# Kernel tuning notes

Hardware: AMD Instinct MI355X
Metric: run time of the kernel (lower is better)

The kernel has to match this reference:

```python
import jax, jax.numpy as jnp
import numpy as np
from jax import lax


def _c1x1(t, w, b=None):
    # t: [B,C,H,W], w: [O,C] (1x1 conv == channel matmul)
    y = jnp.einsum('bchw,oc->bohw', t, w)
    if b is not None:
        y = y + b[None, :, None, None]
    return y


def _mamba(u, in_w, conv_w, conv_b, xproj_w, dt_w, dt_b, A_log, Dp, out_w):
    # u: [B,L,d_model]; Mamba block (mamba_ssm defaults: in/out/x_proj bias=False)
    B, L, _ = u.shape
    d_inner = conv_w.shape[0]
    d_state = A_log.shape[1]
    dt_rank = dt_w.shape[1]
    d_conv = conv_w.shape[2]
    xz = jnp.einsum('bld,ed->ble', u, in_w)          # [B,L,2*d_inner]
    xc, z = xz[..., :d_inner], xz[..., d_inner:]
    # depthwise causal conv1d over seq
    xt = jnp.pad(xc.transpose(0, 2, 1), ((0, 0), (0, 0), (d_conv - 1, 0)))
    xt = lax.conv_general_dilated(xt, conv_w, (1,), 'VALID',
                                  feature_group_count=d_inner,
                                  dimension_numbers=('NCH', 'OIH', 'NCH'))
    xc = jax.nn.silu(xt + conv_b[None, :, None]).transpose(0, 2, 1)  # [B,L,d_inner]
    dbc = jnp.einsum('bld,ed->ble', xc, xproj_w)     # [B,L,dt_rank+2*d_state]
    dt = dbc[..., :dt_rank]
    B_ = dbc[..., dt_rank:dt_rank + d_state]
    C_ = dbc[..., dt_rank + d_state:]
    delta = jax.nn.softplus(jnp.einsum('blr,dr->bld', dt, dt_w) + dt_b)  # [B,L,d_inner]
    A = -jnp.exp(A_log)                              # [d_inner,d_state]
    dA = jnp.exp(delta[..., None] * A)               # [B,L,D,N]
    dBu = delta[..., None] * B_[:, :, None, :] * xc[..., None]
    def step(h, inp):
        dA_t, dBu_t, c_t = inp
        h = dA_t * h + dBu_t                         # [B,D,N]
        y = jnp.einsum('bdn,bn->bd', h, c_t)
        return h, y
    h0 = jnp.zeros((B, d_inner, d_state), dtype=u.dtype)
    _, ys = lax.scan(step, h0, (dA.transpose(1, 0, 2, 3),
                                dBu.transpose(1, 0, 2, 3),
                                C_.transpose(1, 0, 2)))
    y = ys.transpose(1, 0, 2) + xc * Dp              # [B,L,d_inner]
    y = y * jax.nn.silu(z)
    return jnp.einsum('bld,od->blo', y, out_w)       # [B,L,d_model]


def setup_inputs() -> dict:
    key = jax.random.key(0)
    B, C, H, W = 8, 128, 160, 160
    mip, d_in, d_st, d_r, d_cv = 8, 256, 16, 8, 4
    ks = iter(jax.random.split(key, 64))
    def rn(shape, s=0.05):
        return (jax.random.normal(next(ks), shape, dtype=jnp.float32) * s)
    inp = {'x': jax.random.normal(next(ks), (B, C, H, W), dtype=jnp.float32)}
    inp.update(conv1_w=rn((mip, C)), conv1_b=rn((mip,)),
               bn_g=jnp.ones((mip,)), bn_b=jnp.zeros((mip,)),
               bn_m=jnp.zeros((mip,)), bn_v=jnp.ones((mip,)),
               convh_w=rn((C, mip)), convh_b=rn((C,)),
               convw_w=rn((C, mip)), convw_b=rn((C,)),
               mlpx_w1=rn((C, C)), mlpx_b1=rn((C,)), mlpx_w2=rn((C, C)), mlpx_b2=rn((C,)),
               mlpy_w1=rn((C, C)), mlpy_b1=rn((C,)), mlpy_w2=rn((C, C)), mlpy_b2=rn((C,)),
               adjust_w=rn((C, 2 * C)))
    for p in ('mx', 'my'):
        inp[p + '_in_w'] = rn((2 * d_in, C))
        inp[p + '_conv_w'] = rn((d_in, 1, d_cv), 0.3)
        inp[p + '_conv_b'] = rn((d_in,))
        inp[p + '_xproj_w'] = rn((d_r + 2 * d_st, d_in))
        inp[p + '_dt_w'] = rn((d_in, d_r))
        inp[p + '_dt_b'] = rn((d_in,))
        inp[p + '_Alog'] = jnp.log(jnp.broadcast_to(jnp.arange(1, d_st + 1, dtype=jnp.float32), (d_in, d_st)))
        inp[p + '_D'] = jnp.ones((d_in,))
        inp[p + '_out_w'] = rn((C, d_in))
    return inp


def reference(x, conv1_w, conv1_b, bn_g, bn_b, bn_m, bn_v, convh_w, convh_b,
              convw_w, convw_b, mlpx_w1, mlpx_b1, mlpx_w2, mlpx_b2,
              mlpy_w1, mlpy_b1, mlpy_w2, mlpy_b2, adjust_w,
              mx_in_w, mx_conv_w, mx_conv_b, mx_xproj_w, mx_dt_w, mx_dt_b,
              mx_Alog, mx_D, mx_out_w,
              my_in_w, my_conv_w, my_conv_b, my_xproj_w, my_dt_w, my_dt_b,
              my_Alog, my_D, my_out_w):
    B, C, H, W = x.shape
    gelu = lambda t: jax.nn.gelu(t, approximate=False)
    # CoordAttWithMLP
    x_h = x.mean(3, keepdims=True)                      # [B,C,H,1]
    x_w = x.mean(2, keepdims=True).transpose(0, 1, 3, 2)  # [B,C,W,1]
    y = jnp.concatenate([x_h, x_w], axis=2)             # [B,C,H+W,1]
    y = _c1x1(y, conv1_w, conv1_b)
    y = (y - bn_m[None, :, None, None]) * jax.lax.rsqrt(bn_v + 1e-5)[None, :, None, None]
    y = y * bn_g[None, :, None, None] + bn_b[None, :, None, None]
    y = gelu(y)
    a_h = _c1x1(y[:, :, :H], convh_w, convh_b)          # [B,C,H,1] (pre-sigmoid)
    a_w = _c1x1(y[:, :, H:].transpose(0, 1, 3, 2), convw_w, convw_b)  # [B,C,1,W]
    # EfficientMambaAttention00
    ux = x.mean(3).transpose(0, 2, 1)                   # [B,H,C]
    x_x = _mamba(ux, mx_in_w, mx_conv_w, mx_conv_b, mx_xproj_w,
                 mx_dt_w, mx_dt_b, mx_Alog, mx_D, mx_out_w)
    x_x = x_x.transpose(0, 2, 1)[..., None]             # [B,C,H,1]
    x_x = jax.nn.sigmoid(x_x + a_h)
    x_x = _c1x1(gelu(_c1x1(x_x, mlpx_w1, mlpx_b1)), mlpx_w2, mlpx_b2)
    uy = x.mean(2).transpose(0, 2, 1)                   # [B,W,C]
    x_y = _mamba(uy, my_in_w, my_conv_w, my_conv_b, my_xproj_w,
                 my_dt_w, my_dt_b, my_Alog, my_D, my_out_w)
    x_y = x_y.transpose(0, 2, 1)[:, :, None, :]         # [B,C,1,W]
    x_y = jax.nn.sigmoid(x_y + a_w)
    x_y = _c1x1(gelu(_c1x1(x_y, mlpy_w1, mlpy_b1)), mlpy_w2, mlpy_b2)
    # combine
    result_h = jax.nn.sigmoid(a_h) * x_y                # [B,C,H,W]
    result_w = jax.nn.sigmoid(a_w) * x_x                # [B,C,H,W]
    out1 = _c1x1(jnp.concatenate([result_h, result_w], axis=1), adjust_w)
    return x * out1
```

## Files before the change

kernel.cpp:

```cpp
#include <hip/hip_runtime.h>
#include <hip/hip_bf16.h>
#include <math.h>


typedef __attribute__((ext_vector_type(8))) short short8;
typedef __attribute__((ext_vector_type(4))) float f32x4;

__device__ __forceinline__ float sigm_(float x){ return 1.f/(1.f+__expf(-x)); }
__device__ __forceinline__ float silu_(float x){ return x/(1.f+__expf(-x)); }
__device__ __forceinline__ float gelu_(float x){ return 0.5f*x*(1.f+erff(x*0.7071067811865476f)); }
__device__ __forceinline__ float softplus_(float x){ return (x>20.f)?x:log1pf(__expf(x)); }

__global__ void k_means(const float* __restrict__ x, float* __restrict__ xh, float* __restrict__ xw){
  int bc = blockIdx.x;
  const float* xt = x + (size_t)bc*25600;
  int tid = threadIdx.x, wave = tid>>6, lane = tid&63;
  __shared__ float4 colpart[4][40];
  float csx=0.f, csy=0.f, csz=0.f, csw=0.f;
  for (int i=0;i<40;i++){
    int h = wave*40+i;
    float4 v = make_float4(0.f,0.f,0.f,0.f);
    if (lane<40) v = ((const float4*)(xt + h*160))[lane];
    csx+=v.x; csy+=v.y; csz+=v.z; csw+=v.w;
    float r = v.x+v.y+v.z+v.w;
    for (int off=32; off>0; off>>=1) r += __shfl_down(r, off, 64);
    if (lane==0) xh[(size_t)bc*160+h] = r*(1.f/160.f);
  }
  if (lane<40) colpart[wave][lane] = make_float4(csx,csy,csz,csw);
  __syncthreads();
  if (tid<40){
    float4 a=colpart[0][tid], b=colpart[1][tid], c=colpart[2][tid], d=colpart[3][tid];
    float4 s = make_float4((a.x+b.x+c.x+d.x)*(1.f/160.f), (a.y+b.y+c.y+d.y)*(1.f/160.f),
                           (a.z+b.z+c.z+d.z)*(1.f/160.f), (a.w+b.w+c.w+d.w)*(1.f/160.f));
    ((float4*)(xw + (size_t)bc*160))[tid] = s;
  }
}

__global__ void k_ybranch(const float* __restrict__ xh, const float* __restrict__ xw,
                          const float* __restrict__ w1, const float* __restrict__ b1,
                          const float* __restrict__ bg, const float* __restrict__ bb,
                          const float* __restrict__ bm, const float* __restrict__ bv,
                          float* __restrict__ ybuf){
  int gid = blockIdx.x*blockDim.x + threadIdx.x;
  if (gid >= 8*320) return;
  int b = gid/320, p = gid%320;
  const float* in = (p<160) ? (xh + (size_t)b*128*160 + p) : (xw + (size_t)b*128*160 + (p-160));
  float acc[8] = {0,0,0,0,0,0,0,0};
  for (int c=0;c<128;c++){
    float u = in[c*160];
    #pragma unroll
    for (int m=0;m<8;m++) acc[m] += w1[m*128+c]*u;
  }
  #pragma unroll
  for (int m=0;m<8;m++){
    float val = acc[m] + b1[m];
    val = (val - bm[m]) * rsqrtf(bv[m] + 1e-5f);
    val = val * bg[m] + bb[m];
    ybuf[(b*320+p)*8+m] = gelu_(val);
  }
}

__global__ void k_ahw(const float* __restrict__ ybuf,
                      const float* __restrict__ wh, const float* __restrict__ bh,
                      const float* __restrict__ ww, const float* __restrict__ bw,
                      float* __restrict__ a_h, float* __restrict__ a_w){
  int gid = blockIdx.x*blockDim.x + threadIdx.x;
  if (gid >= 8*128*320) return;
  int p = gid%320; int c = (gid/320)%128; int b = gid/(320*128);
  const float* yv = ybuf + (size_t)(b*320+p)*8;
  const float* w = (p<160)? (wh + c*8) : (ww + c*8);
  float acc = (p<160)? bh[c] : bw[c];
  #pragma unroll
  for (int m=0;m<8;m++) acc += w[m]*yv[m];
  if (p<160) a_h[((size_t)(b*128+c))*160+p] = acc;
  else       a_w[((size_t)(b*128+c))*160+(p-160)] = acc;
}

__global__ __launch_bounds__(256) void k_inproj(
                         const float* __restrict__ xh, const float* __restrict__ xw,
                         const float* __restrict__ inw0, const float* __restrict__ inw1,
                         float* __restrict__ xcpre, float* __restrict__ zb){
  __shared__ float uS[8][128];
  int blk = blockIdx.x;
  int g = blk/160, rem = blk%160, b = rem/20, lt = rem%20, lbase = lt*8;
  int t = threadIdx.x;
  const float* src = (g==0)? xh : xw;
  {
    int c = t>>1, lh = t&1;
    float4 v = *(const float4*)(src + ((size_t)(b*128+c))*160 + lbase + lh*4);
    uS[lh*4+0][c]=v.x; uS[lh*4+1][c]=v.y; uS[lh*4+2][c]=v.z; uS[lh*4+3][c]=v.w;
  }
  __syncthreads();
  const float* inw = (g==0)? inw0 : inw1;
  const float* w0p = inw + (size_t)t*128;
  const float* w1p = inw + (size_t)(t+256)*128;
  float acc0[8]={0,0,0,0,0,0,0,0}, acc1[8]={0,0,0,0,0,0,0,0};
  for (int ct=0; ct<16; ct++){
    float4 wa = *(const float4*)(w0p + ct*8);
    float4 wb = *(const float4*)(w0p + ct*8 + 4);
    float4 wc = *(const float4*)(w1p + ct*8);
    float4 wd = *(const float4*)(w1p + ct*8 + 4);
    #pragma unroll
    for (int l=0;l<8;l++){
      float4 ua = *(const float4*)&uS[l][ct*8];
      float4 ub = *(const float4*)&uS[l][ct*8+4];
      acc0[l] += wa.x*ua.x + wa.y*ua.y + wa.z*ua.z + wa.w*ua.w
               + wb.x*ub.x + wb.y*ub.y + wb.z*ub.z + wb.w*ub.w;
      acc1[l] += wc.x*ua.x + wc.y*ua.y + wc.z*ua.z + wc.w*ua.w
               + wd.x*ub.x + wd.y*ub.y + wd.z*ub.z + wd.w*ub.w;
    }
  }
  size_t ob = ((size_t)(g*8+b)*160 + lbase)*256;
  #pragma unroll
  for (int l=0;l<8;l++){
    xcpre[ob + (size_t)l*256 + t] = acc0[l];
    zb   [ob + (size_t)l*256 + t] = acc1[l];
  }
}

__global__ void k_conv(const float* __restrict__ xcpre,
                       const float* __restrict__ cw0, const float* __restrict__ cb0,
                       const float* __restrict__ cw1, const float* __restrict__ cb1,
                       float* __restrict__ xcb){
  int gid = blockIdx.x*blockDim.x + threadIdx.x;
  if (gid >= 2*8*160*256) return;
  int d = gid & 255; int t = gid >> 8; int l = t % 160; int gb = t / 160; int g = gb >> 3;
  const float* cw = ((g==0)? cw0 : cw1) + d*4;
  float acc = ((g==0)? cb0 : cb1)[d];
  const float* base = xcpre + (size_t)gb*160*256 + d;
  #pragma unroll
  for (int k=0;k<4;k++){
    int ls = l-3+k;
    if (ls>=0) acc += cw[k] * base[(size_t)ls*256];
  }
  xcb[gid] = silu_(acc);
}

__global__ void k_prep(const float* __restrict__ adjw, __hip_bfloat16* __restrict__ adjwb){
  int i = blockIdx.x*256 + threadIdx.x;
  if (i < 32768) adjwb[i] = __float2bfloat16(adjw[i]);
}

__global__ __launch_bounds__(256) void k_xproj(
                        const float* __restrict__ xcb,
                        const float* __restrict__ xp0, const float* __restrict__ xp1,
                        float* __restrict__ dbc){
  __shared__ float xv[32][260];
  int blk = blockIdx.x;
  int g = blk/40, rem = blk%40, b = rem/5, lt = rem%5, lbase = lt*32;
  int t = threadIdx.x;
  size_t base = ((size_t)(g*8+b)*160 + lbase)*256;
  for (int i=t; i<8192; i+=256){ int l=i>>8, d=i&255; xv[l][d] = xcb[base+i]; }
  __syncthreads();
  int l = t>>3, s = t&7;
  const float* xp = (g==0)? xp0 : xp1;
  size_t orow = ((size_t)(g*8+b)*160 + lbase + l)*40;
  for (int q=0;q<5;q++){
    int j = s + q*8;
    const float* w = xp + j*256;
    float acc=0.f;
    for (int dd=0; dd<256; dd+=8){
      float4 wa = *(const float4*)(w+dd);
      float4 wb = *(const float4*)(w+dd+4);
      float4 ua = *(const float4*)&xv[l][dd];
      float4 ub = *(const float4*)&xv[l][dd+4];
      acc += wa.x*ua.x + wa.y*ua.y + wa.z*ua.z + wa.w*ua.w
           + wb.x*ub.x + wb.y*ub.y + wb.z*ub.z + wb.w*ub.w;
    }
    dbc[orow + j] = acc;
  }
}

__global__ __launch_bounds__(256) void k_scan(
                       const float* __restrict__ dbc,
                       const float* __restrict__ xcb, const float* __restrict__ zb,
                       const float* __restrict__ dtw0, const float* __restrict__ dtb0,
                       const float* __restrict__ dtw1, const float* __restrict__ dtb1,
                       const float* __restrict__ Alog0, const float* __restrict__ Alog1,
                       const float* __restrict__ D0, const float* __restrict__ D1,
                       float* __restrict__ ysb){
  __shared__ float dsS[160][16];
  __shared__ float BS [160][16];
  __shared__ float CS [160][16];
  __shared__ float xcS[160][16];
  __shared__ float yS [160][16];
  int blk = blockIdx.x;
  int gb = blk >> 4, dblk = blk & 15, g = gb >> 3;
  int dbase = dblk*16;
  int t = threadIdx.x;
  size_t base = (size_t)gb*160*256;
  const float* db = dbc + (size_t)gb*6400;
  const float* dtwG = (g==0)? dtw0 : dtw1;
  const float* dtbG = (g==0)? dtb0 : dtb1;

  #pragma unroll
  for (int i=0;i<10;i++){
    int item = t + 256*i;
    int l = item>>4, c = item&15;
    const float* r = db + l*40;
    int d = dbase + c;
    const float* wt = dtwG + d*8;
    float4 w0 = *(const float4*)wt;
    float4 w1 = *(const float4*)(wt+4);
    float4 r0 = *(const float4*)r;
    float4 r1 = *(const float4*)(r+4);
    float dt = dtbG[d] + w0.x*r0.x+w0.y*r0.y+w0.z*r0.z+w0.w*r0.w
                       + w1.x*r1.x+w1.y*r1.y+w1.z*r1.z+w1.w*r1.w;
    dsS[l][c] = softplus_(dt);
    BS [l][c] = r[8+c];
    CS [l][c] = r[24+c];
    xcS[l][c] = xcb[base + (size_t)l*256 + dbase + c];
  }
  __syncthreads();

  int dloc = t>>4, n = t&15;
  int d = dbase + dloc;
  float A  = -__expf(((g==0)? Alog0 : Alog1)[d*16+n]);
  float Dd = ((g==0)? D0 : D1)[d];
  float h = 0.f;
  for (int lc=0; lc<160; lc+=8){
    float ds8[8], B8[8], C8[8], xc8[8];
    #pragma unroll
    for (int j=0;j<8;j++){
      ds8[j]=dsS[lc+j][dloc]; B8[j]=BS[lc+j][n];
      C8[j]=CS[lc+j][n];      xc8[j]=xcS[lc+j][dloc];
    }
    #pragma unroll
    for (int j=0;j<8;j++){
      float dA = __expf(ds8[j]*A);
      h = dA*h + ds8[j]*B8[j]*xc8[j];
      float p = h*C8[j];
      p += __shfl_xor(p,1,16); p += __shfl_xor(p,2,16);
      p += __shfl_xor(p,4,16); p += __shfl_xor(p,8,16);
      if (n==0) yS[lc+j][dloc] = p + xc8[j]*Dd;
    }
  }
  __syncthreads();

  #pragma unroll
  for (int i=0;i<10;i++){
    int item = t + 256*i;
    int l = item>>4, c = item&15;
    size_t gi = base + (size_t)l*256 + dbase + c;
    ysb[gi] = yS[l][c] * silu_(zb[gi]);
  }
}

__global__ __launch_bounds__(256) void k_post(
                       const float* __restrict__ ysb,
                       const float* __restrict__ ow0, const float* __restrict__ ow1,
                       const float* __restrict__ a_h, const float* __restrict__ a_w,
                       const float* __restrict__ w1x, const float* __restrict__ b1x,
                       const float* __restrict__ w1y, const float* __restrict__ b1y,
                       const float* __restrict__ w2x, const float* __restrict__ b2x,
                       const float* __restrict__ w2y, const float* __restrict__ b2y,
                       float* __restrict__ Qx, float* __restrict__ Qy){
  __shared__ float ysS[10][256];
  __shared__ float Sc[10][128];
  __shared__ float Sp[10][128];
  int blk = blockIdx.x;
  int g = blk>>7, rem = blk&127, b = rem>>4, lt = rem&15, lbase = lt*10;
  int t = threadIdx.x; int c = t&127, kh = t>>7;
  size_t ybase = ((size_t)(g*8+b)*160 + lbase)*256;
  for (int i=t; i<2560; i+=256) ((float*)ysS)[i] = ysb[ybase+i];
  __syncthreads();
  float acc[10];
  {
    const float* w = ((g==0)? ow0 : ow1) + (size_t)c*256 + kh*128;
    #pragma unroll
    for (int l=0;l<10;l++) acc[l]=0.f;
    for (int ct=0; ct<16; ct++){
      float4 wa = *(const float4*)(w + ct*8);
      float4 wb = *(const float4*)(w + ct*8 + 4);
      #pragma unroll
      for (int l=0;l<10;l++){
        float4 ua = *(const float4*)&ysS[l][kh*128+ct*8];
        float4 ub = *(const float4*)&ysS[l][kh*128+ct*8+4];
        acc[l] += wa.x*ua.x + wa.y*ua.y + wa.z*ua.z + wa.w*ua.w
                + wb.x*ub.x + wb.y*ub.y + wb.z*ub.z + wb.w*ub.w;
      }
    }
  }
  if (kh==1){ for (int l=0;l<10;l++) Sc[l][c] = acc[l]; }
  __syncthreads();
  if (kh==0){
    const float* a = ((g==0)? a_h : a_w) + ((size_t)(b*128+c))*160 + lbase;
    #pragma unroll
    for (int l=0;l<10;l++) Sp[l][c] = sigm_(acc[l] + Sc[l][c] + a[l]);
  }
  __syncthreads();
  {
    const float* w = ((g==0)? w1x : w1y) + (size_t)c*128 + kh*64;
    #pragma unroll
    for (int l=0;l<10;l++) acc[l]=0.f;
    for (int ct=0; ct<8; ct++){
      float4 wa = *(const float4*)(w + ct*8);
      float4 wb = *(const float4*)(w + ct*8 + 4);
      #pragma unroll
      for (int l=0;l<10;l++){
        float4 ua = *(const float4*)&Sp[l][kh*64+ct*8];
        float4 ub = *(const float4*)&Sp[l][kh*64+ct*8+4];
        acc[l] += wa.x*ua.x + wa.y*ua.y + wa.z*ua.z + wa.w*ua.w
                + wb.x*ub.x + wb.y*ub.y + wb.z*ub.z + wb.w*ub.w;
      }
    }
  }
  if (kh==1){ for (int l=0;l<10;l++) Sc[l][c] = acc[l]; }
  __syncthreads();
  if (kh==0){
    float bb = ((g==0)? b1x : b1y)[c];
    float tv[10];
    #pragma unroll
    for (int l=0;l<10;l++) tv[l] = gelu_(bb + acc[l] + Sc[l][c]);
    __syncthreads();
    #pragma unroll
    for (int l=0;l<10;l++) Sp[l][c] = tv[l];
  } else {
    __syncthreads();
  }
  __syncthreads();
  {
    const float* w = ((g==0)? w2x : w2y) + (size_t)c*128 + kh*64;
    #pragma unroll
    for (int l=0;l<10;l++) acc[l]=0.f;
    for (int ct=0; ct<8; ct++){
      float4 wa = *(const float4*)(w + ct*8);
      float4 wb = *(const float4*)(w + ct*8 + 4);
      #pragma unroll
      for (int l=0;l<10;l++){
        float4 ua = *(const float4*)&Sp[l][kh*64+ct*8];
        float4 ub = *(const float4*)&Sp[l][kh*64+ct*8+4];
        acc[l] += wa.x*ua.x + wa.y*ua.y + wa.z*ua.z + wa.w*ua.w
                + wb.x*ub.x + wb.y*ub.y + wb.z*ub.z + wb.w*ub.w;
      }
    }
  }
  if (kh==1){ for (int l=0;l<10;l++) Sc[l][c] = acc[l]; }
  __syncthreads();
  if (kh==0){
    float bb = ((g==0)? b2x : b2y)[c];
    float* Q = (g==0)? Qx : Qy;
    size_t orow = ((size_t)(b*128+c))*160 + lbase;
    #pragma unroll
    for (int l=0;l<10;l++) Q[orow + l] = bb + acc[l] + Sc[l][c];
  }
}

__global__ __launch_bounds__(256) void k_final_mfma(
                       const float* __restrict__ x,
                       const float* __restrict__ a_h, const float* __restrict__ a_w,
                       const float* __restrict__ Qx, const float* __restrict__ Qy,
                       const __hip_bfloat16* __restrict__ adjwb, float* __restrict__ out){
  __shared__ __hip_bfloat16 F[80*264];
  int blk = blockIdx.x;
  int b = blk/320; int rem = blk%320; int h = rem>>1; int wh = rem&1;
  int wbase = wh*80;
  int tid = threadIdx.x;
  {
    int k = tid;
    float s;
    const float* rowptr;
    if (k < 128){
      s = sigm_(a_h[((size_t)(b*128+k))*160 + h]);
      rowptr = Qy + ((size_t)(b*128+k))*160 + wbase;
    } else {
      s = Qx[((size_t)(b*128+k-128))*160 + h];
      rowptr = a_w + ((size_t)(b*128+k-128))*160 + wbase;
    }
    const float4* rp4 = (const float4*)rowptr;
    #pragma unroll 4
    for (int u=0; u<20; u++){
      float4 v = rp4[u];
      float f0,f1,f2,f3;
      if (k < 128){ f0=s*v.x; f1=s*v.y; f2=s*v.z; f3=s*v.w; }
      else { f0=s*sigm_(v.x); f1=s*sigm_(v.y); f2=s*sigm_(v.z); f3=s*sigm_(v.w); }
      int wr = u*4;
      F[(wr+0)*264 + k] = __float2bfloat16(f0);
      F[(wr+1)*264 + k] = __float2bfloat16(f1);
      F[(wr+2)*264 + k] = __float2bfloat16(f2);
      F[(wr+3)*264 + k] = __float2bfloat16(f3);
    }
  }
  __syncthreads();

  int wid = tid>>6, lane = tid&63, quad = lane>>4, l16 = lane&15;
  short8 afrag[2][8];
  #pragma unroll
  for (int i=0;i<2;i++){
    int mrow = (wid*2+i)*16 + l16;
    const __hip_bfloat16* ap = adjwb + (size_t)mrow*256 + quad*8;
    #pragma unroll
    for (int kc=0;kc<8;kc++) afrag[i][kc] = *(const short8*)(ap + kc*32);
  }
  for (int nt=0; nt<5; nt++){
    f32x4 acc0 = {0.f,0.f,0.f,0.f}, acc1 = {0.f,0.f,0.f,0.f};
    const __hip_bfloat16* bp = &F[(nt*16 + l16)*264 + quad*8];
    #pragma unroll
    for (int kc=0;kc<8;kc++){
      short8 bf = *(const short8*)(bp + kc*32);
      acc0 = __builtin_amdgcn_mfma_f32_16x16x32_bf16(afrag[0][kc], bf, acc0, 0,0,0);
      acc1 = __builtin_amdgcn_mfma_f32_16x16x32_bf16(afrag[1][kc], bf, acc1, 0,0,0);
    }
    int w = wbase + nt*16 + l16;
    #pragma unroll
    for (int i=0;i<2;i++){
      f32x4 a = i? acc1 : acc0;
      int ob = (wid*2+i)*16 + quad*4;
      #pragma unroll
      for (int r=0;r<4;r++){
        size_t idx = (((size_t)(b*128+ob+r))*160 + h)*160 + w;
        out[idx] = x[idx] * a[r];
      }
    }
  }
}

extern "C" void kernel_launch(void* const* d_in, const int* in_sizes, int n_in,
                              void* d_out, int out_size, void* d_ws, size_t ws_size,
                              hipStream_t stream) {
  #define W(i) ((const float*)d_in[i])
  const float* X = W(0);
  float* ws = (float*)d_ws;
  float* xh    = ws;
  float* xw    = xh    + 163840;
  float* ybuf  = xw    + 163840;
  float* ah    = ybuf  + 20480;
  float* aw    = ah    + 163840;
  float* xcpre = aw    + 163840;
  float* zb    = xcpre + 655360;
  float* xcb   = zb    + 655360;
  float* dbc   = xcb   + 655360;
  float* ysb   = dbc   + 102400;
  float* Qx    = ysb   + 655360;
  float* Qy    = Qx    + 163840;
  __hip_bfloat16* adjwb = (__hip_bfloat16*)xcpre;

  k_means  <<<1024, 256, 0, stream>>>(X, xh, xw);
  k_ybranch<<<10,   256, 0, stream>>>(xh, xw, W(1), W(2), W(3), W(4), W(5), W(6), ybuf);
  k_ahw    <<<1280, 256, 0, stream>>>(ybuf, W(7), W(8), W(9), W(10), ah, aw);
  k_inproj <<<320,  256, 0, stream>>>(xh, xw, W(20), W(29), xcpre, zb);
  k_conv   <<<2560, 256, 0, stream>>>(xcpre, W(21), W(22), W(30), W(31), xcb);
  k_prep   <<<128,  256, 0, stream>>>(W(19), adjwb);
  k_xproj  <<<80,   256, 0, stream>>>(xcb, W(23), W(32), dbc);
  k_scan   <<<256,  256, 0, stream>>>(dbc, xcb, zb, W(24), W(25), W(33), W(34),
                                      W(26), W(35), W(27), W(36), ysb);
  k_post   <<<256,  256, 0, stream>>>(ysb, W(28), W(37), ah, aw,
                                      W(11), W(12), W(15), W(16),
                                      W(13), W(14), W(17), W(18), Qx, Qy);
  k_final_mfma<<<2560, 256, 0, stream>>>(X, ah, aw, Qx, Qy, adjwb, (float*)d_out);
  #undef W
}
```

Measured before the change: 476.2 us.

## Precompute sigmoids and split final MFMA over two K-halves with vectorized stores

k_ahw now also writes sigmoid(a_h) and sigmoid(a_w) to workspace, so the final kernel skips per-element sigmoid evaluation. The final kernel stages the concatenated feature tile in two 128-channel halves, halving shared memory per block. It swaps MFMA operand roles so each lane holds 4 consecutive w outputs, allowing float4 loads of x and float4 stores of out. The k_ahw launch is moved after k_prep because the SH/SW buffers alias the xcpre region, which k_conv reads and k_prep partly overwrites. This adds an extra barrier and more global traffic in k_ahw.

```diff
diff --git a/kernel.cpp b/kernel.cpp
--- a/kernel.cpp
+++ b/kernel.cpp
@@ -63,7 +63,8 @@
 __global__ void k_ahw(const float* __restrict__ ybuf,
                       const float* __restrict__ wh, const float* __restrict__ bh,
                       const float* __restrict__ ww, const float* __restrict__ bw,
-                      float* __restrict__ a_h, float* __restrict__ a_w){
+                      float* __restrict__ a_h, float* __restrict__ a_w,
+                      float* __restrict__ SH, float* __restrict__ SW){
   int gid = blockIdx.x*blockDim.x + threadIdx.x;
   if (gid >= 8*128*320) return;
   int p = gid%320; int c = (gid/320)%128; int b = gid/(320*128);
@@ -72,8 +73,13 @@
   float acc = (p<160)? bh[c] : bw[c];
   #pragma unroll
   for (int m=0;m<8;m++) acc += w[m]*yv[m];
-  if (p<160) a_h[((size_t)(b*128+c))*160+p] = acc;
-  else       a_w[((size_t)(b*128+c))*160+(p-160)] = acc;
+  if (p<160){
+    size_t o = ((size_t)(b*128+c))*160+p;
+    a_h[o] = acc; SH[o] = sigm_(acc);
+  } else {
+    size_t o = ((size_t)(b*128+c))*160+(p-160);
+    a_w[o] = acc; SW[o] = sigm_(acc);
+  }
 }
 
 __global__ __launch_bounds__(256) void k_inproj(
@@ -348,69 +354,73 @@
 
 __global__ __launch_bounds__(256) void k_final_mfma(
                        const float* __restrict__ x,
-                       const float* __restrict__ a_h, const float* __restrict__ a_w,
+                       const float* __restrict__ SH, const float* __restrict__ SW,
                        const float* __restrict__ Qx, const float* __restrict__ Qy,
                        const __hip_bfloat16* __restrict__ adjwb, float* __restrict__ out){
-  __shared__ __hip_bfloat16 F[80*264];
+  __shared__ __hip_bfloat16 F[80*136];
   int blk = blockIdx.x;
   int b = blk/320; int rem = blk%320; int h = rem>>1; int wh = rem&1;
   int wbase = wh*80;
   int tid = threadIdx.x;
-  {
-    int k = tid;
-    float s;
-    const float* rowptr;
-    if (k < 128){
-      s = sigm_(a_h[((size_t)(b*128+k))*160 + h]);
-      rowptr = Qy + ((size_t)(b*128+k))*160 + wbase;
-    } else {
-      s = Qx[((size_t)(b*128+k-128))*160 + h];
-      rowptr = a_w + ((size_t)(b*128+k-128))*160 + wbase;
-    }
-    const float4* rp4 = (const float4*)rowptr;
-    #pragma unroll 4
-    for (int u=0; u<20; u++){
-      float4 v = rp4[u];
-      float f0,f1,f2,f3;
-      if (k < 128){ f0=s*v.x; f1=s*v.y; f2=s*v.z; f3=s*v.w; }
-      else { f0=s*sigm_(v.x); f1=s*sigm_(v.y); f2=s*sigm_(v.z); f3=s*sigm_(v.w); }
-      int wr = u*4;
-      F[(wr+0)*264 + k] = __float2bfloat16(f0);
-      F[(wr+1)*264 + k] = __float2bfloat16(f1);
-      F[(wr+2)*264 + k] = __float2bfloat16(f2);
-      F[(wr+3)*264 + k] = __float2bfloat16(f3);
-    }
-  }
-  __syncthreads();
-
+  int kq = tid & 127, whh = tid >> 7;
   int wid = tid>>6, lane = tid&63, quad = lane>>4, l16 = lane&15;
-  short8 afrag[2][8];
+
+  f32x4 acc[2][5];
+  #pragma unroll
+  for (int i=0;i<2;i++)
+    #pragma unroll
+    for (int nt=0;nt<5;nt++) acc[i][nt] = (f32x4){0.f,0.f,0.f,0.f};
+
+  #pragma unroll
+  for (int ch=0; ch<2; ch++){
+    {
+      size_t rowoff = ((size_t)(b*128+kq))*160;
+      float s;
+      const float* rp;
+      if (ch==0){ s = SH[rowoff + h]; rp = Qy + rowoff + wbase + whh*40; }
+      else      { s = Qx[rowoff + h]; rp = SW + rowoff + wbase + whh*40; }
+      const float4* rp4 = (const float4*)rp;
+      #pragma unroll
+      for (int u=0; u<10; u++){
+        float4 v = rp4[u];
+        int wr = whh*40 + u*4;
+        F[(wr+0)*136 + kq] = __float2bfloat16(s*v.x);
+        F[(wr+1)*136 + kq] = __float2bfloat16(s*v.y);
+        F[(wr+2)*136 + kq] = __float2bfloat16(s*v.z);
+        F[(wr+3)*136 + kq] = __float2bfloat16(s*v.w);
+      }
+    }
+    __syncthreads();
+    short8 bfrag[2][4];
+    #pragma unroll
+    for (int i=0;i<2;i++){
+      const __hip_bfloat16* bp = adjwb + (size_t)((wid*2+i)*16 + l16)*256 + ch*128 + quad*8;
+      #pragma unroll
+      for (int kc=0;kc<4;kc++) bfrag[i][kc] = *(const short8*)(bp + kc*32);
+    }
+    #pragma unroll
+    for (int nt=0; nt<5; nt++){
+      const __hip_bfloat16* ap = &F[(nt*16 + l16)*136 + quad*8];
+      #pragma unroll
+      for (int kc=0;kc<4;kc++){
+        short8 af = *(const short8*)(ap + kc*32);
+        acc[0][nt] = __builtin_amdgcn_mfma_f32_16x16x32_bf16(af, bfrag[0][kc], acc[0][nt], 0,0,0);
+        acc[1][nt] = __builtin_amdgcn_mfma_f32_16x16x32_bf16(af, bfrag[1][kc], acc[1][nt], 0,0,0);
+      }
+    }
+    if (ch==0) __syncthreads();
+  }
   #pragma unroll
   for (int i=0;i<2;i++){
-    int mrow = (wid*2+i)*16 + l16;
-    const __hip_bfloat16* ap = adjwb + (size_t)mrow*256 + quad*8;
-    #pragma unroll
-    for (int kc=0;kc<8;kc++) afrag[i][kc] = *(const short8*)(ap + kc*32);
-  }
-  for (int nt=0; nt<5; nt++){
-    f32x4 acc0 = {0.f,0.f,0.f,0.f}, acc1 = {0.f,0.f,0.f,0.f};
-    const __hip_bfloat16* bp = &F[(nt*16 + l16)*264 + quad*8];
-    #pragma unroll
-    for (int kc=0;kc<8;kc++){
-      short8 bf = *(const short8*)(bp + kc*32);
-      acc0 = __builtin_amdgcn_mfma_f32_16x16x32_bf16(afrag[0][kc], bf, acc0, 0,0,0);
-      acc1 = __builtin_amdgcn_mfma_f32_16x16x32_bf16(afrag[1][kc], bf, acc1, 0,0,0);
-    }
-    int w = wbase + nt*16 + l16;
-    #pragma unroll
-    for (int i=0;i<2;i++){
-      f32x4 a = i? acc1 : acc0;
-      int ob = (wid*2+i)*16 + quad*4;
-      #pragma unroll
-      for (int r=0;r<4;r++){
-        size_t idx = (((size_t)(b*128+ob+r))*160 + h)*160 + w;
-        out[idx] = x[idx] * a[r];
-      }
+    int o = (wid*2+i)*16 + l16;
+    size_t rowb = (((size_t)(b*128+o))*160 + h)*160;
+    #pragma unroll
+    for (int nt=0; nt<5; nt++){
+      int w0 = wbase + nt*16 + quad*4;
+      float4 xv = *(const float4*)(x + rowb + w0);
+      f32x4 a = acc[i][nt];
+      float4 ov = make_float4(xv.x*a[0], xv.y*a[1], xv.z*a[2], xv.w*a[3]);
+      *(float4*)(out + rowb + w0) = ov;
     }
   }
 }
@@ -434,19 +444,21 @@
   float* Qx    = ysb   + 655360;
   float* Qy    = Qx    + 163840;
   __hip_bfloat16* adjwb = (__hip_bfloat16*)xcpre;
+  float* SH    = xcpre + 16384;
+  float* SW    = SH    + 163840;
 
   k_means  <<<1024, 256, 0, stream>>>(X, xh, xw);
   k_ybranch<<<10,   256, 0, stream>>>(xh, xw, W(1), W(2), W(3), W(4), W(5), W(6), ybuf);
-  k_ahw    <<<1280, 256, 0, stream>>>(ybuf, W(7), W(8), W(9), W(10), ah, aw);
   k_inproj <<<320,  256, 0, stream>>>(xh, xw, W(20), W(29), xcpre, zb);
   k_conv   <<<2560, 256, 0, stream>>>(xcpre, W(21), W(22), W(30), W(31), xcb);
   k_prep   <<<128,  256, 0, stream>>>(W(19), adjwb);
+  k_ahw    <<<1280, 256, 0, stream>>>(ybuf, W(7), W(8), W(9), W(10), ah, aw, SH, SW);
   k_xproj  <<<80,   256, 0, stream>>>(xcb, W(23), W(32), dbc);
   k_scan   <<<256,  256, 0, stream>>>(dbc, xcb, zb, W(24), W(25), W(33), W(34),
                                       W(26), W(35), W(27), W(36), ysb);
   k_post   <<<256,  256, 0, stream>>>(ysb, W(28), W(37), ah, aw,
                                       W(11), W(12), W(15), W(16),
                                       W(13), W(14), W(17), W(18), Qx, Qy);
-  k_final_mfma<<<2560, 256, 0, stream>>>(X, ah, aw, Qx, Qy, adjwb, (float*)d_out);
+  k_final_mfma<<<2560, 256, 0, stream>>>(X, SH, SW, Qx, Qy, adjwb, (float*)d_out);
   #undef W
 }
```

Result: no change. 466.9 us (-2.0%).
